# Optimization experiments

Measured on AMD Instinct MI355X. Metric: run time of the kernel, lower is better.

## Reference

```python
import jax, jax.numpy as jnp
import numpy as np

NUM_CLASSES = 1000
FEAT_DIM = 2048
BATCH = 16384


def setup_inputs() -> dict:
    key = jax.random.key(0)
    k1, k2 = jax.random.split(key)
    features = jax.random.normal(k1, (BATCH, FEAT_DIM), dtype=jnp.float32)
    labels = jax.random.randint(k2, (BATCH,), 0, NUM_CLASSES, dtype=jnp.int64)
    return {"features": features, "labels": labels}


def _scatters(features, labels):
    # Faithful to the original (note: cosine_dist is 1 - dot/||u|| * ||v||,
    # reproducing the original operator precedence).
    N = features.shape[0]
    C = NUM_CLASSES
    counts = jax.ops.segment_sum(jnp.ones((N,), features.dtype), labels, num_segments=C)  # [C]
    sums = jax.ops.segment_sum(features, labels, num_segments=C)                          # [C, D]
    means = jnp.nan_to_num(sums / counts[:, None])  # per-class means, empty class -> 0
    overall = jnp.mean(features, axis=0)            # [D]

    def cdist(U, v):
        # U: [..., D], v: [D]; matches torch: 1 - dot(u,v)/||u|| * ||v||
        return 1.0 - (U @ v) / jnp.linalg.norm(U, axis=-1) * jnp.linalg.norm(v)

    # St: mean squared cosine-distance of each sample to the overall mean (scalar)
    st = (cdist(features, overall) ** 2).sum() / N

    # Sb (weighted): sum_c Ni/N * dist(mean_c, overall)^2 (scalar)
    d_mb = cdist(means, overall) ** 2                # [C]
    sb = ((counts / N) * d_mb).sum()

    # Sw (weighted): per class, (1/Ni) * sum_{i in c} dist(x_i, mean_c)^2, scaled by Ni/N
    row_mean = means[labels]                         # [N, D]
    d = 1.0 - jnp.einsum('nd,nd->n', features, row_mean) \
        / jnp.linalg.norm(features, axis=-1) * jnp.linalg.norm(row_mean, axis=-1)
    per_class = jax.ops.segment_sum(d ** 2, labels, num_segments=C)  # [C]
    sw_list = (1.0 / counts) * per_class * (counts / N)              # [C]
    return st, sw_list, sb


def reference(features, labels):
    st, sw_list, sb = _scatters(features, labels)
    sw = jnp.mean(sw_list)        # forward: Sw_t = mean(Sw_t, dim=0)
    sb_t = st - sw                # forward: Sb_t = St_t - Sw_t
    return jnp.stack([st, sw, sb_t])
```

## Files before the change

### kernel.cpp

```cpp
#include <hip/hip_runtime.h>
#include <math.h>

#define N_SAMPLES 16384
#define FEAT 2048
#define NCLS 1000
#define CPAD 1024
#define MAIN_BLOCKS 2048


__global__ void hist_kernel(const int* __restrict__ labels, int* __restrict__ counts) {
  int i = blockIdx.x * blockDim.x + threadIdx.x;
  if (i < N_SAMPLES) atomicAdd(&counts[labels[i]], 1);
}

__global__ void scan_kernel(const int* __restrict__ counts, int* __restrict__ offsets,
                            int* __restrict__ cursor) {
  __shared__ int buf0[CPAD], buf1[CPAD];
  int t = threadIdx.x;
  buf0[t] = counts[t];
  __syncthreads();
  int* src = buf0;
  int* dst = buf1;
  for (int off = 1; off < CPAD; off <<= 1) {
    dst[t] = src[t] + (t >= off ? src[t - off] : 0);
    __syncthreads();
    int* tmp = src; src = dst; dst = tmp;
  }
  int excl = (t == 0) ? 0 : src[t - 1];
  offsets[t] = excl;
  cursor[t] = excl;
}

__global__ void scatter_kernel(const int* __restrict__ labels, int* __restrict__ cursor,
                               int* __restrict__ perm) {
  int i = blockIdx.x * blockDim.x + threadIdx.x;
  if (i < N_SAMPLES) {
    int pos = atomicAdd(&cursor[labels[i]], 1);
    perm[pos] = i;
  }
}

__global__ __launch_bounds__(256) void class_sum_kernel(
    const float* __restrict__ feat, const int* __restrict__ offsets,
    const int* __restrict__ counts, const int* __restrict__ perm,
    float* __restrict__ sums, float* __restrict__ snorm) {
  const int c = blockIdx.x, t = threadIdx.x;
  const int beg = offsets[c], n = counts[c];
  float a0 = 0, a1 = 0, a2 = 0, a3 = 0, b0 = 0, b1 = 0, b2 = 0, b3 = 0;
  int r = 0;
  for (; r + 4 <= n; r += 4) {
    const float4* r0 = (const float4*)(feat + (size_t)perm[beg + r] * FEAT);
    const float4* r1 = (const float4*)(feat + (size_t)perm[beg + r + 1] * FEAT);
    const float4* r2 = (const float4*)(feat + (size_t)perm[beg + r + 2] * FEAT);
    const float4* r3 = (const float4*)(feat + (size_t)perm[beg + r + 3] * FEAT);
    float4 v0 = r0[t], w0 = r0[t + 256];
    float4 v1 = r1[t], w1 = r1[t + 256];
    float4 v2 = r2[t], w2 = r2[t + 256];
    float4 v3 = r3[t], w3 = r3[t + 256];
    a0 += (v0.x + v1.x) + (v2.x + v3.x);
    a1 += (v0.y + v1.y) + (v2.y + v3.y);
    a2 += (v0.z + v1.z) + (v2.z + v3.z);
    a3 += (v0.w + v1.w) + (v2.w + v3.w);
    b0 += (w0.x + w1.x) + (w2.x + w3.x);
    b1 += (w0.y + w1.y) + (w2.y + w3.y);
    b2 += (w0.z + w1.z) + (w2.z + w3.z);
    b3 += (w0.w + w1.w) + (w2.w + w3.w);
  }
  for (; r < n; ++r) {
    const float4* r0 = (const float4*)(feat + (size_t)perm[beg + r] * FEAT);
    float4 v0 = r0[t], w0 = r0[t + 256];
    a0 += v0.x; a1 += v0.y; a2 += v0.z; a3 += v0.w;
    b0 += w0.x; b1 += w0.y; b2 += w0.z; b3 += w0.w;
  }
  float4* sr = (float4*)(sums + (size_t)c * FEAT);
  sr[t] = make_float4(a0, a1, a2, a3);
  sr[t + 256] = make_float4(b0, b1, b2, b3);
  float sq = a0 * a0 + a1 * a1 + a2 * a2 + a3 * a3 +
             b0 * b0 + b1 * b1 + b2 * b2 + b3 * b3;
  for (int off = 32; off; off >>= 1) sq += __shfl_xor(sq, off);
  __shared__ float red[4];
  int w = t >> 6, lane = t & 63;
  if (lane == 0) red[w] = sq;
  __syncthreads();
  if (t == 0) snorm[c] = sqrtf(red[0] + red[1] + red[2] + red[3]);
}

__global__ __launch_bounds__(256) void overall_part_kernel(
    const float* __restrict__ sums, float* __restrict__ part_ov) {
  int dchunk = blockIdx.x & 7;
  int cchunk = blockIdx.x >> 3;
  int d = dchunk * 256 + threadIdx.x;
  float acc = 0.f;
  int cbeg = cchunk * 125, cend = cbeg + 125;
  for (int c = cbeg; c < cend; ++c) acc += sums[(size_t)c * FEAT + d];
  part_ov[cchunk * FEAT + d] = acc;
}

__global__ __launch_bounds__(256) void ovnorm_kernel(
    const float* __restrict__ part_ov, float* __restrict__ overall,
    float* __restrict__ scalars) {
  int t = threadIdx.x;
  float sq = 0.f;
  for (int k = 0; k < 8; ++k) {
    int d = t + 256 * k;
    float v = 0.f;
    for (int p = 0; p < 8; ++p) v += part_ov[p * FEAT + d];
    overall[d] = v;
    sq += v * v;
  }
  for (int off = 32; off; off >>= 1) sq += __shfl_xor(sq, off);
  __shared__ float red[4];
  int w = t >> 6, lane = t & 63;
  if (lane == 0) red[w] = sq;
  __syncthreads();
  if (t == 0) scalars[0] = sqrtf(red[0] + red[1] + red[2] + red[3]);
}

__global__ __launch_bounds__(256) void main_kernel(
    const float* __restrict__ feat, const int* __restrict__ labels,
    const float* __restrict__ sums, const float* __restrict__ snorm,
    const float* __restrict__ overall, const int* __restrict__ counts,
    const float* __restrict__ scalars, float* __restrict__ pst,
    float* __restrict__ psw) {
  const int t = threadIdx.x, w = t >> 6, lane = t & 63;
  const float4* ov = (const float4*)overall;
  const float invN2 = 1.f / ((float)N_SAMPLES * (float)N_SAMPLES);
  const float ovn = scalars[0];
  float st_acc = 0.f, sw_acc = 0.f;
#pragma unroll
  for (int rep = 0; rep < 2; ++rep) {
    const int row = blockIdx.x * 4 + w + rep * (MAIN_BLOCKS * 4);
    const int l = labels[row];
    const float4* xr = (const float4*)(feat + (size_t)row * FEAT);
    const float4* srw = (const float4*)(sums + (size_t)l * FEAT);
    float dxo = 0.f, dxs = 0.f, nx2 = 0.f;
#pragma unroll
    for (int k = 0; k < 8; ++k) {
      float4 x = xr[lane + 64 * k];
      float4 s = srw[lane + 64 * k];
      float4 o = ov[lane + 64 * k];
      dxo += x.x * o.x + x.y * o.y + x.z * o.z + x.w * o.w;
      dxs += x.x * s.x + x.y * s.y + x.z * s.z + x.w * s.w;
      nx2 += x.x * x.x + x.y * x.y + x.z * x.z + x.w * x.w;
    }
    for (int off = 32; off; off >>= 1) {
      dxo += __shfl_xor(dxo, off);
      dxs += __shfl_xor(dxs, off);
      nx2 += __shfl_xor(nx2, off);
    }
    if (lane == 0) {
      float nx = sqrtf(nx2);
      float cnt = (float)counts[l];
      float t1 = 1.f - dxo * ovn * invN2 / nx;
      float t2 = 1.f - dxs * snorm[l] / (cnt * cnt * nx);
      st_acc += t1 * t1;
      sw_acc += t2 * t2;
    }
  }
  __shared__ float red[8];
  if (lane == 0) { red[w] = st_acc; red[4 + w] = sw_acc; }
  __syncthreads();
  if (t == 0) {
    pst[blockIdx.x] = red[0] + red[1] + red[2] + red[3];
    psw[blockIdx.x] = red[4] + red[5] + red[6] + red[7];
  }
}

__global__ __launch_bounds__(1024) void final_kernel(
    const float* __restrict__ pst, const float* __restrict__ psw,
    float* __restrict__ out) {
  int t = threadIdx.x;
  float st = pst[t] + pst[t + 1024];
  float sw = psw[t] + psw[t + 1024];
  for (int off = 32; off; off >>= 1) {
    st += __shfl_xor(st, off);
    sw += __shfl_xor(sw, off);
  }
  __shared__ float rs[16], rw[16];
  int w = t >> 6, lane = t & 63;
  if (lane == 0) { rs[w] = st; rw[w] = sw; }
  __syncthreads();
  if (t == 0) {
    float s = 0.f, q = 0.f;
    for (int i = 0; i < 16; ++i) { s += rs[i]; q += rw[i]; }
    float stv = s / (float)N_SAMPLES;
    float swv = q / ((float)N_SAMPLES * (float)NCLS);
    out[0] = stv;
    out[1] = swv;
    out[2] = stv - swv;
  }
}

extern "C" void kernel_launch(void* const* d_in, const int* in_sizes, int n_in,
                              void* d_out, int out_size, void* d_ws, size_t ws_size,
                              hipStream_t stream) {
  const float* feat = (const float*)d_in[0];
  const int* labels = (const int*)d_in[1];
  float* out = (float*)d_out;

  float* sums = (float*)d_ws;
  float* snorm = sums + (size_t)NCLS * FEAT;
  float* overall = snorm + CPAD;
  float* part_ov = overall + FEAT;
  float* pst = part_ov + 8 * FEAT;
  float* psw = pst + MAIN_BLOCKS;
  int* counts = (int*)(psw + MAIN_BLOCKS);
  float* scalars = (float*)(counts + CPAD);
  int* offsets = (int*)(scalars + 4);
  int* cursor = offsets + CPAD;
  int* perm = cursor + CPAD;

  hipMemsetAsync(counts, 0, (CPAD + 4) * sizeof(int), stream);
  hist_kernel<<<64, 256, 0, stream>>>(labels, counts);
  scan_kernel<<<1, 1024, 0, stream>>>(counts, offsets, cursor);
  scatter_kernel<<<64, 256, 0, stream>>>(labels, cursor, perm);
  class_sum_kernel<<<NCLS, 256, 0, stream>>>(feat, offsets, counts, perm, sums, snorm);
  overall_part_kernel<<<64, 256, 0, stream>>>(sums, part_ov);
  ovnorm_kernel<<<1, 256, 0, stream>>>(part_ov, overall, scalars);
  main_kernel<<<MAIN_BLOCKS, 256, 0, stream>>>(feat, labels, sums, snorm, overall,
                                               counts, scalars, pst, psw);
  final_kernel<<<1, 1024, 0, stream>>>(pst, psw, out);
}
```

Measured before the change: 94.08 us.

## Fuse histogram/scan/scatter into one block and fold overall-norm via last-block

Replaces the separate histogram, scan and scatter kernels (plus a memset) with a single 1024-thread kernel that builds the class histogram in shared memory, scans it and writes the permutation. It also merges the overall-mean reduction and its norm into one kernel, using a threadfence and an atomic counter so the last block finishes the work. Separately, main_kernel now runs one row per wave with twice as many blocks. Together these cut the number of kernel launches and the small serial kernels between them, at the cost of a single-block sort stage and atomic-based synchronisation between blocks.

```diff
diff --git a/kernel.cpp b/kernel.cpp
--- a/kernel.cpp
+++ b/kernel.cpp
@@ -5,38 +5,50 @@
 #define FEAT 2048
 #define NCLS 1000
 #define CPAD 1024
-#define MAIN_BLOCKS 2048
-
-
-__global__ void hist_kernel(const int* __restrict__ labels, int* __restrict__ counts) {
-  int i = blockIdx.x * blockDim.x + threadIdx.x;
-  if (i < N_SAMPLES) atomicAdd(&counts[labels[i]], 1);
-}
-
-__global__ void scan_kernel(const int* __restrict__ counts, int* __restrict__ offsets,
-                            int* __restrict__ cursor) {
-  __shared__ int buf0[CPAD], buf1[CPAD];
-  int t = threadIdx.x;
-  buf0[t] = counts[t];
-  __syncthreads();
-  int* src = buf0;
-  int* dst = buf1;
+#define MAIN_BLOCKS 4096
+
+
+__global__ __launch_bounds__(1024) void sort_kernel(
+    const int* __restrict__ labels, int* __restrict__ counts,
+    int* __restrict__ offsets, int* __restrict__ perm) {
+  __shared__ int h[CPAD];
+  __shared__ int buf[CPAD];
+  const int t = threadIdx.x;
+  h[t] = 0;
+  __syncthreads();
+  int4 q[4];
+  const int4* lb = (const int4*)(labels + t * 16);
+#pragma unroll
+  for (int j = 0; j < 4; ++j) q[j] = lb[j];
+#pragma unroll
+  for (int j = 0; j < 4; ++j) {
+    atomicAdd(&h[q[j].x], 1);
+    atomicAdd(&h[q[j].y], 1);
+    atomicAdd(&h[q[j].z], 1);
+    atomicAdd(&h[q[j].w], 1);
+  }
+  __syncthreads();
+  counts[t] = h[t];
+  int* src = h;
+  int* dst = buf;
   for (int off = 1; off < CPAD; off <<= 1) {
     dst[t] = src[t] + (t >= off ? src[t - off] : 0);
     __syncthreads();
     int* tmp = src; src = dst; dst = tmp;
   }
-  int excl = (t == 0) ? 0 : src[t - 1];
+  const int excl = (t == 0) ? 0 : src[t - 1];
   offsets[t] = excl;
-  cursor[t] = excl;
-}
-
-__global__ void scatter_kernel(const int* __restrict__ labels, int* __restrict__ cursor,
-                               int* __restrict__ perm) {
-  int i = blockIdx.x * blockDim.x + threadIdx.x;
-  if (i < N_SAMPLES) {
-    int pos = atomicAdd(&cursor[labels[i]], 1);
-    perm[pos] = i;
+  __syncthreads();
+  dst[t] = excl;
+  __syncthreads();
+#pragma unroll
+  for (int j = 0; j < 4; ++j) {
+    int idx = t * 16 + 4 * j;
+    int p;
+    p = atomicAdd(&dst[q[j].x], 1); perm[p] = idx;
+    p = atomicAdd(&dst[q[j].y], 1); perm[p] = idx + 1;
+    p = atomicAdd(&dst[q[j].z], 1); perm[p] = idx + 2;
+    p = atomicAdd(&dst[q[j].w], 1); perm[p] = idx + 3;
   }
 }
 
@@ -85,35 +97,40 @@
   if (t == 0) snorm[c] = sqrtf(red[0] + red[1] + red[2] + red[3]);
 }
 
-__global__ __launch_bounds__(256) void overall_part_kernel(
-    const float* __restrict__ sums, float* __restrict__ part_ov) {
-  int dchunk = blockIdx.x & 7;
-  int cchunk = blockIdx.x >> 3;
-  int d = dchunk * 256 + threadIdx.x;
+__global__ __launch_bounds__(256) void overall_kernel(
+    const float* __restrict__ sums, float* __restrict__ part_ov,
+    float* __restrict__ overall, float* __restrict__ scalars,
+    int* __restrict__ done) {
+  const int dchunk = blockIdx.x & 7;
+  const int cchunk = blockIdx.x >> 3;
+  const int t = threadIdx.x;
+  const int d = dchunk * 256 + t;
   float acc = 0.f;
-  int cbeg = cchunk * 125, cend = cbeg + 125;
+  const int cbeg = cchunk * 125, cend = cbeg + 125;
   for (int c = cbeg; c < cend; ++c) acc += sums[(size_t)c * FEAT + d];
   part_ov[cchunk * FEAT + d] = acc;
-}
-
-__global__ __launch_bounds__(256) void ovnorm_kernel(
-    const float* __restrict__ part_ov, float* __restrict__ overall,
-    float* __restrict__ scalars) {
-  int t = threadIdx.x;
-  float sq = 0.f;
-  for (int k = 0; k < 8; ++k) {
-    int d = t + 256 * k;
-    float v = 0.f;
-    for (int p = 0; p < 8; ++p) v += part_ov[p * FEAT + d];
-    overall[d] = v;
-    sq += v * v;
-  }
-  for (int off = 32; off; off >>= 1) sq += __shfl_xor(sq, off);
-  __shared__ float red[4];
-  int w = t >> 6, lane = t & 63;
-  if (lane == 0) red[w] = sq;
-  __syncthreads();
-  if (t == 0) scalars[0] = sqrtf(red[0] + red[1] + red[2] + red[3]);
+  __threadfence();
+  __shared__ int lastv;
+  if (t == 0) lastv = atomicAdd(done, 1);
+  __syncthreads();
+  if (lastv == 63) {
+    __threadfence();
+    float sq = 0.f;
+    for (int k = 0; k < 8; ++k) {
+      int dd = t + 256 * k;
+      float v = 0.f;
+#pragma unroll
+      for (int p = 0; p < 8; ++p) v += part_ov[p * FEAT + dd];
+      overall[dd] = v;
+      sq += v * v;
+    }
+    for (int off = 32; off; off >>= 1) sq += __shfl_xor(sq, off);
+    __shared__ float red[4];
+    int w = t >> 6, lane = t & 63;
+    if (lane == 0) red[w] = sq;
+    __syncthreads();
+    if (t == 0) scalars[0] = sqrtf(red[0] + red[1] + red[2] + red[3]);
+  }
 }
 
 __global__ __launch_bounds__(256) void main_kernel(
@@ -126,36 +143,33 @@
   const float4* ov = (const float4*)overall;
   const float invN2 = 1.f / ((float)N_SAMPLES * (float)N_SAMPLES);
   const float ovn = scalars[0];
+  const int row = blockIdx.x * 4 + w;
+  const int l = labels[row];
+  const float4* xr = (const float4*)(feat + (size_t)row * FEAT);
+  const float4* srw = (const float4*)(sums + (size_t)l * FEAT);
+  float dxo = 0.f, dxs = 0.f, nx2 = 0.f;
+#pragma unroll
+  for (int k = 0; k < 8; ++k) {
+    float4 x = xr[lane + 64 * k];
+    float4 s = srw[lane + 64 * k];
+    float4 o = ov[lane + 64 * k];
+    dxo += x.x * o.x + x.y * o.y + x.z * o.z + x.w * o.w;
+    dxs += x.x * s.x + x.y * s.y + x.z * s.z + x.w * s.w;
+    nx2 += x.x * x.x + x.y * x.y + x.z * x.z + x.w * x.w;
+  }
+  for (int off = 32; off; off >>= 1) {
+    dxo += __shfl_xor(dxo, off);
+    dxs += __shfl_xor(dxs, off);
+    nx2 += __shfl_xor(nx2, off);
+  }
   float st_acc = 0.f, sw_acc = 0.f;
-#pragma unroll
-  for (int rep = 0; rep < 2; ++rep) {
-    const int row = blockIdx.x * 4 + w + rep * (MAIN_BLOCKS * 4);
-    const int l = labels[row];
-    const float4* xr = (const float4*)(feat + (size_t)row * FEAT);
-    const float4* srw = (const float4*)(sums + (size_t)l * FEAT);
-    float dxo = 0.f, dxs = 0.f, nx2 = 0.f;
-#pragma unroll
-    for (int k = 0; k < 8; ++k) {
-      float4 x = xr[lane + 64 * k];
-      float4 s = srw[lane + 64 * k];
-      float4 o = ov[lane + 64 * k];
-      dxo += x.x * o.x + x.y * o.y + x.z * o.z + x.w * o.w;
-      dxs += x.x * s.x + x.y * s.y + x.z * s.z + x.w * s.w;
-      nx2 += x.x * x.x + x.y * x.y + x.z * x.z + x.w * x.w;
-    }
-    for (int off = 32; off; off >>= 1) {
-      dxo += __shfl_xor(dxo, off);
-      dxs += __shfl_xor(dxs, off);
-      nx2 += __shfl_xor(nx2, off);
-    }
-    if (lane == 0) {
-      float nx = sqrtf(nx2);
-      float cnt = (float)counts[l];
-      float t1 = 1.f - dxo * ovn * invN2 / nx;
-      float t2 = 1.f - dxs * snorm[l] / (cnt * cnt * nx);
-      st_acc += t1 * t1;
-      sw_acc += t2 * t2;
-    }
+  if (lane == 0) {
+    float nx = sqrtf(nx2);
+    float cnt = (float)counts[l];
+    float t1 = 1.f - dxo * ovn * invN2 / nx;
+    float t2 = 1.f - dxs * snorm[l] / (cnt * cnt * nx);
+    st_acc = t1 * t1;
+    sw_acc = t2 * t2;
   }
   __shared__ float red[8];
   if (lane == 0) { red[w] = st_acc; red[4 + w] = sw_acc; }
@@ -170,8 +184,12 @@
     const float* __restrict__ pst, const float* __restrict__ psw,
     float* __restrict__ out) {
   int t = threadIdx.x;
-  float st = pst[t] + pst[t + 1024];
-  float sw = psw[t] + psw[t + 1024];
+  float st = 0.f, sw = 0.f;
+#pragma unroll
+  for (int k = 0; k < MAIN_BLOCKS / 1024; ++k) {
+    st += pst[t + 1024 * k];
+    sw += psw[t + 1024 * k];
+  }
   for (int off = 32; off; off >>= 1) {
     st += __shfl_xor(st, off);
     sw += __shfl_xor(sw, off);
@@ -204,19 +222,16 @@
   float* part_ov = overall + FEAT;
   float* pst = part_ov + 8 * FEAT;
   float* psw = pst + MAIN_BLOCKS;
-  int* counts = (int*)(psw + MAIN_BLOCKS);
-  float* scalars = (float*)(counts + CPAD);
-  int* offsets = (int*)(scalars + 4);
-  int* cursor = offsets + CPAD;
-  int* perm = cursor + CPAD;
-
-  hipMemsetAsync(counts, 0, (CPAD + 4) * sizeof(int), stream);
-  hist_kernel<<<64, 256, 0, stream>>>(labels, counts);
-  scan_kernel<<<1, 1024, 0, stream>>>(counts, offsets, cursor);
-  scatter_kernel<<<64, 256, 0, stream>>>(labels, cursor, perm);
+  float* scalars = psw + MAIN_BLOCKS;
+  int* counts = (int*)(scalars + 4);
+  int* offsets = counts + CPAD;
+  int* perm = offsets + CPAD;
+  int* done = perm + N_SAMPLES;
+
+  hipMemsetAsync(done, 0, 16 * sizeof(int), stream);
+  sort_kernel<<<1, 1024, 0, stream>>>(labels, counts, offsets, perm);
   class_sum_kernel<<<NCLS, 256, 0, stream>>>(feat, offsets, counts, perm, sums, snorm);
-  overall_part_kernel<<<64, 256, 0, stream>>>(sums, part_ov);
-  ovnorm_kernel<<<1, 256, 0, stream>>>(part_ov, overall, scalars);
+  overall_kernel<<<64, 256, 0, stream>>>(sums, part_ov, overall, scalars, done);
   main_kernel<<<MAIN_BLOCKS, 256, 0, stream>>>(feat, labels, sums, snorm, overall,
                                                counts, scalars, pst, psw);
   final_kernel<<<1, 1024, 0, stream>>>(pst, psw, out);
```

Measured after the change: 95.53 us. About the same (+1.5%).

## Fuse class sums with per-sample distance pass and merge sort into column-sum kernel

Applied to the files above, without the earlier changes.

Replaces the nine-launch pipeline with four kernels. Block 0 of the first kernel builds the histogram, scan and permutation in shared memory while the other blocks compute column partial sums of all features for the overall mean. A per-class kernel then accumulates the class sum into LDS and immediately re-reads its rows to compute both distances, which removes the global sums buffer and the separate main pass. The features are still read twice, and the class-sum block now depends on a MAXCLS=320 cap on class size, so an unusually large class would overflow the shared permutation buffer.

```diff
diff --git a/kernel.cpp b/kernel.cpp
--- a/kernel.cpp
+++ b/kernel.cpp
@@ -5,140 +5,193 @@
 #define FEAT 2048
 #define NCLS 1000
 #define CPAD 1024
-#define MAIN_BLOCKS 2048
-
-
-__global__ void hist_kernel(const int* __restrict__ labels, int* __restrict__ counts) {
-  int i = blockIdx.x * blockDim.x + threadIdx.x;
-  if (i < N_SAMPLES) atomicAdd(&counts[labels[i]], 1);
-}
-
-__global__ void scan_kernel(const int* __restrict__ counts, int* __restrict__ offsets,
-                            int* __restrict__ cursor) {
-  __shared__ int buf0[CPAD], buf1[CPAD];
-  int t = threadIdx.x;
-  buf0[t] = counts[t];
+#define MAXCLS 320
+#define NCOLS 256
+#define ROWS_PER_COL (N_SAMPLES / NCOLS)
+
+
+__global__ __launch_bounds__(256) void k1_sort_colsum(
+    const int* __restrict__ labels, const float* __restrict__ feat,
+    int* __restrict__ counts, int* __restrict__ offsets, int* __restrict__ perm,
+    float* __restrict__ part_ov) {
+  const int t = threadIdx.x, lane = t & 63, w = t >> 6;
+  if (blockIdx.x == 0) {
+    __shared__ int h[CPAD];
+    __shared__ int cur[CPAD];
+    __shared__ int wtot[4];
+    for (int i = t; i < CPAD; i += 256) h[i] = 0;
+    __syncthreads();
+    const int4* lb = (const int4*)labels;
+    for (int j = t; j < N_SAMPLES / 4; j += 256) {
+      int4 q = lb[j];
+      atomicAdd(&h[q.x], 1);
+      atomicAdd(&h[q.y], 1);
+      atomicAdd(&h[q.z], 1);
+      atomicAdd(&h[q.w], 1);
+    }
+    __syncthreads();
+    const int b4 = 4 * t;
+    const int e0 = h[b4], e1 = h[b4 + 1], e2 = h[b4 + 2], e3 = h[b4 + 3];
+    const int ssum = e0 + e1 + e2 + e3;
+    int v = ssum;
+    for (int off = 1; off < 64; off <<= 1) {
+      int p = __shfl_up(v, off);
+      if (lane >= off) v += p;
+    }
+    if (lane == 63) wtot[w] = v;
+    __syncthreads();
+    int wb = 0;
+    for (int i = 0; i < w; ++i) wb += wtot[i];
+    const int excl = wb + v - ssum;
+    counts[b4] = e0; counts[b4 + 1] = e1; counts[b4 + 2] = e2; counts[b4 + 3] = e3;
+    offsets[b4] = excl;
+    offsets[b4 + 1] = excl + e0;
+    offsets[b4 + 2] = excl + e0 + e1;
+    offsets[b4 + 3] = excl + e0 + e1 + e2;
+    cur[b4] = excl;
+    cur[b4 + 1] = excl + e0;
+    cur[b4 + 2] = excl + e0 + e1;
+    cur[b4 + 3] = excl + e0 + e1 + e2;
+    __syncthreads();
+    for (int j = t; j < N_SAMPLES / 4; j += 256) {
+      int4 q = lb[j];
+      int idx = 4 * j;
+      int p0 = atomicAdd(&cur[q.x], 1); perm[p0] = idx;
+      int p1 = atomicAdd(&cur[q.y], 1); perm[p1] = idx + 1;
+      int p2 = atomicAdd(&cur[q.z], 1); perm[p2] = idx + 2;
+      int p3 = atomicAdd(&cur[q.w], 1); perm[p3] = idx + 3;
+    }
+  } else {
+    const int bb = blockIdx.x - 1;
+    const float4* f4 = (const float4*)feat;
+    const size_t rowbase = (size_t)bb * ROWS_PER_COL;
+    float a0 = 0, a1 = 0, a2 = 0, a3 = 0, b0 = 0, b1 = 0, b2 = 0, b3 = 0;
+    for (int r = 0; r < ROWS_PER_COL; r += 4) {
+      const float4* p0 = f4 + (rowbase + r) * 512;
+      const float4* p1 = f4 + (rowbase + r + 1) * 512;
+      const float4* p2 = f4 + (rowbase + r + 2) * 512;
+      const float4* p3 = f4 + (rowbase + r + 3) * 512;
+      float4 v0 = p0[t], u0 = p0[t + 256];
+      float4 v1 = p1[t], u1 = p1[t + 256];
+      float4 v2 = p2[t], u2 = p2[t + 256];
+      float4 v3 = p3[t], u3 = p3[t + 256];
+      a0 += (v0.x + v1.x) + (v2.x + v3.x);
+      a1 += (v0.y + v1.y) + (v2.y + v3.y);
+      a2 += (v0.z + v1.z) + (v2.z + v3.z);
+      a3 += (v0.w + v1.w) + (v2.w + v3.w);
+      b0 += (u0.x + u1.x) + (u2.x + u3.x);
+      b1 += (u0.y + u1.y) + (u2.y + u3.y);
+      b2 += (u0.z + u1.z) + (u2.z + u3.z);
+      b3 += (u0.w + u1.w) + (u2.w + u3.w);
+    }
+    float4* o4 = (float4*)part_ov;
+    o4[bb * 512 + t] = make_float4(a0, a1, a2, a3);
+    o4[bb * 512 + t + 256] = make_float4(b0, b1, b2, b3);
+  }
+}
+
+__global__ __launch_bounds__(256) void k2_fold(const float* __restrict__ part_ov,
+                                               float* __restrict__ overall) {
+  const float4* p4 = (const float4*)part_ov;
+  const int t = threadIdx.x;
+  const int fi = blockIdx.x * 32 + (t & 31);
+  const int g = t >> 5;
+  float a0 = 0, a1 = 0, a2 = 0, a3 = 0;
+  for (int b = g; b < NCOLS; b += 8) {
+    float4 v = p4[b * 512 + fi];
+    a0 += v.x; a1 += v.y; a2 += v.z; a3 += v.w;
+  }
+  __shared__ float4 lds[8][32];
+  lds[g][t & 31] = make_float4(a0, a1, a2, a3);
   __syncthreads();
-  int* src = buf0;
-  int* dst = buf1;
-  for (int off = 1; off < CPAD; off <<= 1) {
-    dst[t] = src[t] + (t >= off ? src[t - off] : 0);
-    __syncthreads();
-    int* tmp = src; src = dst; dst = tmp;
-  }
-  int excl = (t == 0) ? 0 : src[t - 1];
-  offsets[t] = excl;
-  cursor[t] = excl;
-}
-
-__global__ void scatter_kernel(const int* __restrict__ labels, int* __restrict__ cursor,
-                               int* __restrict__ perm) {
-  int i = blockIdx.x * blockDim.x + threadIdx.x;
-  if (i < N_SAMPLES) {
-    int pos = atomicAdd(&cursor[labels[i]], 1);
-    perm[pos] = i;
-  }
-}
-
-__global__ __launch_bounds__(256) void class_sum_kernel(
+  if (g == 0) {
+    float s0 = 0, s1 = 0, s2 = 0, s3 = 0;
+#pragma unroll
+    for (int i = 0; i < 8; ++i) {
+      float4 v = lds[i][t];
+      s0 += v.x; s1 += v.y; s2 += v.z; s3 += v.w;
+    }
+    ((float4*)overall)[fi] = make_float4(s0, s1, s2, s3);
+  }
+}
+
+__global__ __launch_bounds__(256) void k3_class_pass(
     const float* __restrict__ feat, const int* __restrict__ offsets,
     const int* __restrict__ counts, const int* __restrict__ perm,
-    float* __restrict__ sums, float* __restrict__ snorm) {
-  const int c = blockIdx.x, t = threadIdx.x;
+    const float* __restrict__ overall, float* __restrict__ pst,
+    float* __restrict__ psw) {
+  const int c = blockIdx.x, t = threadIdx.x, w = t >> 6, lane = t & 63;
+  __shared__ int lperm[MAXCLS];
+  __shared__ float sums_lds[FEAT];
+  __shared__ float red[4];
+  __shared__ float sc[2];
   const int beg = offsets[c], n = counts[c];
+  for (int i = t; i < n; i += 256) lperm[i] = perm[beg + i];
+
+  const float4* ov4 = (const float4*)overall;
+  {
+    float4 o1 = ov4[t], o2 = ov4[t + 256];
+    float sq = o1.x * o1.x + o1.y * o1.y + o1.z * o1.z + o1.w * o1.w +
+               o2.x * o2.x + o2.y * o2.y + o2.z * o2.z + o2.w * o2.w;
+    for (int off = 32; off; off >>= 1) sq += __shfl_xor(sq, off);
+    if (lane == 0) red[w] = sq;
+    __syncthreads();
+    if (t == 0) sc[1] = sqrtf(red[0] + red[1] + red[2] + red[3]);
+  }
+
+  const float4* f4 = (const float4*)feat;
   float a0 = 0, a1 = 0, a2 = 0, a3 = 0, b0 = 0, b1 = 0, b2 = 0, b3 = 0;
   int r = 0;
   for (; r + 4 <= n; r += 4) {
-    const float4* r0 = (const float4*)(feat + (size_t)perm[beg + r] * FEAT);
-    const float4* r1 = (const float4*)(feat + (size_t)perm[beg + r + 1] * FEAT);
-    const float4* r2 = (const float4*)(feat + (size_t)perm[beg + r + 2] * FEAT);
-    const float4* r3 = (const float4*)(feat + (size_t)perm[beg + r + 3] * FEAT);
-    float4 v0 = r0[t], w0 = r0[t + 256];
-    float4 v1 = r1[t], w1 = r1[t + 256];
-    float4 v2 = r2[t], w2 = r2[t + 256];
-    float4 v3 = r3[t], w3 = r3[t + 256];
+    const float4* p0 = f4 + (size_t)lperm[r] * 512;
+    const float4* p1 = f4 + (size_t)lperm[r + 1] * 512;
+    const float4* p2 = f4 + (size_t)lperm[r + 2] * 512;
+    const float4* p3 = f4 + (size_t)lperm[r + 3] * 512;
+    float4 v0 = p0[t], u0 = p0[t + 256];
+    float4 v1 = p1[t], u1 = p1[t + 256];
+    float4 v2 = p2[t], u2 = p2[t + 256];
+    float4 v3 = p3[t], u3 = p3[t + 256];
     a0 += (v0.x + v1.x) + (v2.x + v3.x);
     a1 += (v0.y + v1.y) + (v2.y + v3.y);
     a2 += (v0.z + v1.z) + (v2.z + v3.z);
     a3 += (v0.w + v1.w) + (v2.w + v3.w);
-    b0 += (w0.x + w1.x) + (w2.x + w3.x);
-    b1 += (w0.y + w1.y) + (w2.y + w3.y);
-    b2 += (w0.z + w1.z) + (w2.z + w3.z);
-    b3 += (w0.w + w1.w) + (w2.w + w3.w);
+    b0 += (u0.x + u1.x) + (u2.x + u3.x);
+    b1 += (u0.y + u1.y) + (u2.y + u3.y);
+    b2 += (u0.z + u1.z) + (u2.z + u3.z);
+    b3 += (u0.w + u1.w) + (u2.w + u3.w);
   }
   for (; r < n; ++r) {
-    const float4* r0 = (const float4*)(feat + (size_t)perm[beg + r] * FEAT);
-    float4 v0 = r0[t], w0 = r0[t + 256];
-    a0 += v0.x; a1 += v0.y; a2 += v0.z; a3 += v0.w;
-    b0 += w0.x; b1 += w0.y; b2 += w0.z; b3 += w0.w;
-  }
-  float4* sr = (float4*)(sums + (size_t)c * FEAT);
-  sr[t] = make_float4(a0, a1, a2, a3);
-  sr[t + 256] = make_float4(b0, b1, b2, b3);
-  float sq = a0 * a0 + a1 * a1 + a2 * a2 + a3 * a3 +
-             b0 * b0 + b1 * b1 + b2 * b2 + b3 * b3;
-  for (int off = 32; off; off >>= 1) sq += __shfl_xor(sq, off);
-  __shared__ float red[4];
-  int w = t >> 6, lane = t & 63;
-  if (lane == 0) red[w] = sq;
-  __syncthreads();
-  if (t == 0) snorm[c] = sqrtf(red[0] + red[1] + red[2] + red[3]);
-}
-
-__global__ __launch_bounds__(256) void overall_part_kernel(
-    const float* __restrict__ sums, float* __restrict__ part_ov) {
-  int dchunk = blockIdx.x & 7;
-  int cchunk = blockIdx.x >> 3;
-  int d = dchunk * 256 + threadIdx.x;
-  float acc = 0.f;
-  int cbeg = cchunk * 125, cend = cbeg + 125;
-  for (int c = cbeg; c < cend; ++c) acc += sums[(size_t)c * FEAT + d];
-  part_ov[cchunk * FEAT + d] = acc;
-}
-
-__global__ __launch_bounds__(256) void ovnorm_kernel(
-    const float* __restrict__ part_ov, float* __restrict__ overall,
-    float* __restrict__ scalars) {
-  int t = threadIdx.x;
-  float sq = 0.f;
-  for (int k = 0; k < 8; ++k) {
-    int d = t + 256 * k;
-    float v = 0.f;
-    for (int p = 0; p < 8; ++p) v += part_ov[p * FEAT + d];
-    overall[d] = v;
-    sq += v * v;
-  }
-  for (int off = 32; off; off >>= 1) sq += __shfl_xor(sq, off);
-  __shared__ float red[4];
-  int w = t >> 6, lane = t & 63;
-  if (lane == 0) red[w] = sq;
-  __syncthreads();
-  if (t == 0) scalars[0] = sqrtf(red[0] + red[1] + red[2] + red[3]);
-}
-
-__global__ __launch_bounds__(256) void main_kernel(
-    const float* __restrict__ feat, const int* __restrict__ labels,
-    const float* __restrict__ sums, const float* __restrict__ snorm,
-    const float* __restrict__ overall, const int* __restrict__ counts,
-    const float* __restrict__ scalars, float* __restrict__ pst,
-    float* __restrict__ psw) {
-  const int t = threadIdx.x, w = t >> 6, lane = t & 63;
-  const float4* ov = (const float4*)overall;
+    const float4* p0 = f4 + (size_t)lperm[r] * 512;
+    float4 v = p0[t], u = p0[t + 256];
+    a0 += v.x; a1 += v.y; a2 += v.z; a3 += v.w;
+    b0 += u.x; b1 += u.y; b2 += u.z; b3 += u.w;
+  }
+  float4* s4 = (float4*)sums_lds;
+  s4[t] = make_float4(a0, a1, a2, a3);
+  s4[t + 256] = make_float4(b0, b1, b2, b3);
+  {
+    float sq = a0 * a0 + a1 * a1 + a2 * a2 + a3 * a3 +
+               b0 * b0 + b1 * b1 + b2 * b2 + b3 * b3;
+    for (int off = 32; off; off >>= 1) sq += __shfl_xor(sq, off);
+    __syncthreads();
+    if (lane == 0) red[w] = sq;
+    __syncthreads();
+    if (t == 0) sc[0] = sqrtf(red[0] + red[1] + red[2] + red[3]);
+    __syncthreads();
+  }
+
+  const float snormv = sc[0], ovn = sc[1];
   const float invN2 = 1.f / ((float)N_SAMPLES * (float)N_SAMPLES);
-  const float ovn = scalars[0];
+  const float cnt = (float)n;
   float st_acc = 0.f, sw_acc = 0.f;
-#pragma unroll
-  for (int rep = 0; rep < 2; ++rep) {
-    const int row = blockIdx.x * 4 + w + rep * (MAIN_BLOCKS * 4);
-    const int l = labels[row];
-    const float4* xr = (const float4*)(feat + (size_t)row * FEAT);
-    const float4* srw = (const float4*)(sums + (size_t)l * FEAT);
+  for (int rr = w; rr < n; rr += 4) {
+    const float4* xr = f4 + (size_t)lperm[rr] * 512;
     float dxo = 0.f, dxs = 0.f, nx2 = 0.f;
 #pragma unroll
     for (int k = 0; k < 8; ++k) {
       float4 x = xr[lane + 64 * k];
-      float4 s = srw[lane + 64 * k];
-      float4 o = ov[lane + 64 * k];
+      float4 s = s4[lane + 64 * k];
+      float4 o = ov4[lane + 64 * k];
       dxo += x.x * o.x + x.y * o.y + x.z * o.z + x.w * o.w;
       dxs += x.x * s.x + x.y * s.y + x.z * s.z + x.w * s.w;
       nx2 += x.x * x.x + x.y * x.y + x.z * x.z + x.w * x.w;
@@ -150,39 +203,37 @@
     }
     if (lane == 0) {
       float nx = sqrtf(nx2);
-      float cnt = (float)counts[l];
       float t1 = 1.f - dxo * ovn * invN2 / nx;
-      float t2 = 1.f - dxs * snorm[l] / (cnt * cnt * nx);
+      float t2 = 1.f - dxs * snormv / (cnt * cnt * nx);
       st_acc += t1 * t1;
       sw_acc += t2 * t2;
     }
   }
-  __shared__ float red[8];
-  if (lane == 0) { red[w] = st_acc; red[4 + w] = sw_acc; }
+  __shared__ float red2[8];
+  if (lane == 0) { red2[w] = st_acc; red2[4 + w] = sw_acc; }
   __syncthreads();
   if (t == 0) {
-    pst[blockIdx.x] = red[0] + red[1] + red[2] + red[3];
-    psw[blockIdx.x] = red[4] + red[5] + red[6] + red[7];
-  }
-}
-
-__global__ __launch_bounds__(1024) void final_kernel(
-    const float* __restrict__ pst, const float* __restrict__ psw,
-    float* __restrict__ out) {
-  int t = threadIdx.x;
-  float st = pst[t] + pst[t + 1024];
-  float sw = psw[t] + psw[t + 1024];
+    pst[c] = red2[0] + red2[1] + red2[2] + red2[3];
+    psw[c] = red2[4] + red2[5] + red2[6] + red2[7];
+  }
+}
+
+__global__ __launch_bounds__(256) void k4_final(const float* __restrict__ pst,
+                                                const float* __restrict__ psw,
+                                                float* __restrict__ out) {
+  const int t = threadIdx.x, w = t >> 6, lane = t & 63;
+  float st = 0.f, sw = 0.f;
+  for (int i = t; i < NCLS; i += 256) { st += pst[i]; sw += psw[i]; }
   for (int off = 32; off; off >>= 1) {
     st += __shfl_xor(st, off);
     sw += __shfl_xor(sw, off);
   }
-  __shared__ float rs[16], rw[16];
-  int w = t >> 6, lane = t & 63;
+  __shared__ float rs[4], rw[4];
   if (lane == 0) { rs[w] = st; rw[w] = sw; }
   __syncthreads();
   if (t == 0) {
-    float s = 0.f, q = 0.f;
-    for (int i = 0; i < 16; ++i) { s += rs[i]; q += rw[i]; }
+    float s = rs[0] + rs[1] + rs[2] + rs[3];
+    float q = rw[0] + rw[1] + rw[2] + rw[3];
     float stv = s / (float)N_SAMPLES;
     float swv = q / ((float)N_SAMPLES * (float)NCLS);
     out[0] = stv;
@@ -198,26 +249,18 @@
   const int* labels = (const int*)d_in[1];
   float* out = (float*)d_out;
 
-  float* sums = (float*)d_ws;
-  float* snorm = sums + (size_t)NCLS * FEAT;
-  float* overall = snorm + CPAD;
-  float* part_ov = overall + FEAT;
-  float* pst = part_ov + 8 * FEAT;
-  float* psw = pst + MAIN_BLOCKS;
-  int* counts = (int*)(psw + MAIN_BLOCKS);
-  float* scalars = (float*)(counts + CPAD);
-  int* offsets = (int*)(scalars + 4);
-  int* cursor = offsets + CPAD;
-  int* perm = cursor + CPAD;
-
-  hipMemsetAsync(counts, 0, (CPAD + 4) * sizeof(int), stream);
-  hist_kernel<<<64, 256, 0, stream>>>(labels, counts);
-  scan_kernel<<<1, 1024, 0, stream>>>(counts, offsets, cursor);
-  scatter_kernel<<<64, 256, 0, stream>>>(labels, cursor, perm);
-  class_sum_kernel<<<NCLS, 256, 0, stream>>>(feat, offsets, counts, perm, sums, snorm);
-  overall_part_kernel<<<64, 256, 0, stream>>>(sums, part_ov);
-  ovnorm_kernel<<<1, 256, 0, stream>>>(part_ov, overall, scalars);
-  main_kernel<<<MAIN_BLOCKS, 256, 0, stream>>>(feat, labels, sums, snorm, overall,
-                                               counts, scalars, pst, psw);
-  final_kernel<<<1, 1024, 0, stream>>>(pst, psw, out);
-}
+  float* part_ov = (float*)d_ws;
+  float* overall = part_ov + NCOLS * FEAT;
+  float* pst = overall + FEAT;
+  float* psw = pst + CPAD;
+  int* counts = (int*)(psw + CPAD);
+  int* offsets = counts + CPAD;
+  int* perm = offsets + CPAD;
+
+  k1_sort_colsum<<<NCOLS + 1, 256, 0, stream>>>(labels, feat, counts, offsets, perm,
+                                                part_ov);
+  k2_fold<<<16, 256, 0, stream>>>(part_ov, overall);
+  k3_class_pass<<<NCLS, 256, 0, stream>>>(feat, offsets, counts, perm, overall, pst,
+                                          psw);
+  k4_final<<<1, 256, 0, stream>>>(pst, psw, out);
+}
```

Result: no change. 95.33 us (+1.3%).
